# Performance work log

Measured on AMD Instinct MI355X. Metric: run time of the kernel, lower is better.

## Reference

```python
import jax, jax.numpy as jnp
import numpy as np

N_USERS = 60000
N_ITEMS = 40000
N_NODES = N_USERS + N_ITEMS
N_EDGES = 1_000_000
D = 64
BN_EPS = 1e-3  # tf.layers.batch_normalization default epsilon


def setup_inputs() -> dict:
    key = jax.random.key(0)
    ks = jax.random.split(key, 16)
    s = 1.0 / np.sqrt(D)  # uniform-ish init scale for [D,D] weights
    w = lambda k: (jax.random.uniform(k, (D, D), jnp.float32, -1.0, 1.0) * s)
    return {
        "u_features": jax.random.normal(ks[0], (N_USERS, D), jnp.float32),
        "v_features": jax.random.normal(ks[1], (N_ITEMS, D), jnp.float32),
        "edge_start": jax.random.randint(ks[2], (N_EDGES,), 0, N_NODES, jnp.int32),
        "edge_end": jax.random.randint(ks[3], (N_EDGES,), 0, N_NODES, jnp.int32),
        "Ui1": w(ks[4]), "Uj1": w(ks[5]), "Vi1": w(ks[6]), "Vj1": w(ks[7]),
        "bu1": jnp.zeros((D,), jnp.float32), "bv1": jnp.zeros((D,), jnp.float32),
        "Ui2": w(ks[8]), "Uj2": w(ks[9]), "Vi2": w(ks[10]), "Vj2": w(ks[11]),
        "bu2": jnp.zeros((D,), jnp.float32), "bv2": jnp.zeros((D,), jnp.float32),
        "R": w(ks[12]),
        "gamma1": jnp.ones((D,), jnp.float32), "beta1": jnp.zeros((D,), jnp.float32),
        "gamma2": jnp.ones((D,), jnp.float32), "beta2": jnp.zeros((D,), jnp.float32),
    }


def _stage(x, Ui, Uj, Vi, Vj, bu, bv, e_start, e_end, n_nodes):
    # gate = sigmoid(E_end@(x Vi) + E_start@(x Vj) + bv)   -> edge gather
    gate = jax.nn.sigmoid((x @ Vi)[e_end] + (x @ Vj)[e_start] + bv)  # [E, D]
    msg = gate * (x @ Ui)[e_start]                                    # [E, D]
    # x Uj + E_end.T @ msg + bu   -> scatter-add to destination nodes
    agg = jax.ops.segment_sum(msg, e_end, num_segments=n_nodes)       # [N, D]
    return x @ Uj + agg + bu


def _batchnorm(x, gamma, beta):
    mean = jnp.mean(x, axis=0)
    var = jnp.var(x, axis=0)
    return gamma * (x - mean) * jax.lax.rsqrt(var + BN_EPS) + beta


def reference(u_features, v_features, edge_start, edge_end,
              Ui1, Uj1, Vi1, Vj1, bu1, bv1,
              Ui2, Uj2, Vi2, Vj2, bu2, bv2,
              R, gamma1, beta1, gamma2, beta2):
    num_users = u_features.shape[0]
    x_in = jnp.concatenate([u_features, v_features], axis=0)  # [N, D]
    n = x_in.shape[0]
    x = _stage(x_in, Ui1, Uj1, Vi1, Vj1, bu1, bv1, edge_start, edge_end, n)
    x = jax.nn.relu(_batchnorm(x, gamma1, beta1))
    x = _stage(x, Ui2, Uj2, Vi2, Vj2, bu2, bv2, edge_start, edge_end, n)
    x = _batchnorm(x, gamma2, beta2)
    x = jax.nn.relu(x + x_in @ R)  # residual branch
    return x[:num_users], x[num_users:]
```

## Files before the change

kernel.cpp:

```cpp
#include <hip/hip_runtime.h>
#include <hip/hip_bf16.h>

#define NUSERS 60000
#define NNODES 100000
#define DD 64
#define NGB 1563
#define GMM 782
#define NBUK 196
#define ESB 2048

typedef __hip_bfloat16 bf16;
using bf16x8 = __attribute__((ext_vector_type(8))) short;
using f32x4  = __attribute__((ext_vector_type(4))) float;

__device__ __forceinline__ float b2f(bf16 x) { return __bfloat162float(x); }
__device__ __forceinline__ bf16 f2b(float x) { return __float2bfloat16(x); }
__device__ __forceinline__ unsigned short fbits(float x) {
    union { bf16 b; unsigned short u; } cv; cv.b = f2b(x); return cv.u;
}
__device__ __forceinline__ float us2f(unsigned short h) {
    union { unsigned u; float f; } t; t.u = (unsigned)h << 16; return t.f;
}
__device__ __forceinline__ float lo_bf16(unsigned w) {
    union { unsigned u; float f; } t; t.u = w << 16; return t.f;
}
__device__ __forceinline__ float hi_bf16(unsigned w) {
    union { unsigned u; float f; } t; t.u = w & 0xFFFF0000u; return t.f;
}
__device__ __forceinline__ float ldf(const void* p, size_t i, int isbf) {
    if (isbf) return b2f(((const bf16*)p)[i]);
    return ((const float*)p)[i];
}
__device__ __forceinline__ unsigned pack2(float a, float b) {
    return (unsigned)fbits(a) | ((unsigned)fbits(b) << 16);
}
__device__ __forceinline__ unsigned pr2(float x0, float x1, float a0, float a1,
                                        float b0, float b1) {
    float t0 = a0 * x0 + b0, t1 = a1 * x1 + b1;
    t0 = t0 > 0.f ? t0 : 0.f;
    t1 = t1 > 0.f ? t1 : 0.f;
    return pack2(t0, t1);
}

__global__ void k_sniff(const unsigned short* __restrict__ h,
                        int* __restrict__ flag, float* __restrict__ red,
                        int* __restrict__ btot)
{
    __shared__ int cs[256];
    int t = threadIdx.x;
    int cnt = 0;
    for (int i = t; i < 1024; i += 256) {
        int e = (h[2 * i] >> 7) & 0xFF;
        cnt += (e >= 100 && e <= 140) ? 1 : 0;
    }
    cs[t] = cnt;
    __syncthreads();
    for (int s = 128; s > 0; s >>= 1) {
        if (t < s) cs[t] += cs[t + s];
        __syncthreads();
    }
    if (t == 0) flag[0] = (cs[0] > 512) ? 1 : 0;
    red[t] = 0.f;
    btot[t] = 0;
}

__global__ __launch_bounds__(256) void k_bhist(const int* __restrict__ ee,
                                               int* __restrict__ btot, int E)
{
    __shared__ int h[256];
    int t = threadIdx.x;
    h[t] = 0;
    __syncthreads();
    for (int e = blockIdx.x * 256 + t; e < E; e += gridDim.x * 256)
        atomicAdd(&h[ee[e] >> 9], 1);
    __syncthreads();
    if (h[t]) atomicAdd(&btot[t], h[t]);
}

__global__ void k_bscan(const int* __restrict__ btot, int* __restrict__ bbase,
                        int* __restrict__ bcursor)
{
    __shared__ int sd[256];
    int t = threadIdx.x;
    int v = btot[t];
    sd[t] = v;
    __syncthreads();
    for (int off = 1; off < 256; off <<= 1) {
        int x = (t >= off) ? sd[t - off] : 0;
        __syncthreads();
        sd[t] += x;
        __syncthreads();
    }
    int excl = sd[t] - v;
    bbase[t] = excl;
    bcursor[t] = excl;
}

__global__ __launch_bounds__(256) void k_bscatter(
    const int* __restrict__ es, const int* __restrict__ ee,
    int* __restrict__ bcursor, unsigned* __restrict__ ebuf, int E)
{
    __shared__ int h[256], gb[256], lr[256];
    int t = threadIdx.x;
    h[t] = 0;
    lr[t] = 0;
    __syncthreads();
    int base = blockIdx.x * ESB;
    unsigned ent[8];
    int bk[8];
#pragma unroll
    for (int i = 0; i < 8; i++) {
        int e = base + t + i * 256;
        if (e < E) {
            int s = es[e], d = ee[e];
            bk[i] = d >> 9;
            ent[i] = (unsigned)s | ((unsigned)(d & 511) << 20);
            atomicAdd(&h[bk[i]], 1);
        } else bk[i] = -1;
    }
    __syncthreads();
    if (h[t]) gb[t] = atomicAdd(&bcursor[t], h[t]);
    __syncthreads();
#pragma unroll
    for (int i = 0; i < 8; i++) {
        if (bk[i] >= 0) {
            int r = atomicAdd(&lr[bk[i]], 1);
            ebuf[gb[bk[i]] + r] = ent[i];
        }
    }
}

__global__ __launch_bounds__(256) void k_group(
    const int* __restrict__ bbase, const unsigned* __restrict__ ebuf,
    int* __restrict__ rowptr, int* __restrict__ srcidx)
{
    __shared__ int h[512], sc[512];
    int b = blockIdx.x, t = threadIdx.x;
    int lo = bbase[b], hi = bbase[b + 1];
    h[t] = 0;
    h[t + 256] = 0;
    __syncthreads();
    for (int i = lo + t; i < hi; i += 256)
        atomicAdd(&h[ebuf[i] >> 20], 1);
    __syncthreads();
    sc[t] = h[t];
    sc[t + 256] = h[t + 256];
    __syncthreads();
    for (int off = 1; off < 512; off <<= 1) {
        int v0 = (t >= off) ? sc[t - off] : 0;
        int v1 = (t + 256 >= off) ? sc[t + 256 - off] : 0;
        __syncthreads();
        sc[t] += v0;
        sc[t + 256] += v1;
        __syncthreads();
    }
    int n0 = b * 512 + t, n1 = b * 512 + t + 256;
    int e0 = lo + sc[t] - h[t];
    int e1 = lo + sc[t + 256] - h[t + 256];
    if (n0 < NNODES) rowptr[n0] = e0;
    if (n1 < NNODES) rowptr[n1] = e1;
    if (b == NBUK - 1 && t == 0) rowptr[NNODES] = hi;
    h[t] = e0;
    h[t + 256] = e1;
    __syncthreads();
    for (int i = lo + t; i < hi; i += 256) {
        unsigned en = ebuf[i];
        int pos = atomicAdd(&h[en >> 20], 1);
        int s = (int)(en & 0xFFFFF);
        srcidx[pos] = s < NNODES ? s : 0;
    }
}

template <int MODE>
__device__ __forceinline__ void stage_load(
    int tile, int tid, int bfflag,
    const void* u, const void* v, const unsigned short* Aacc,
    const float* ab, uint4& w0, uint4& w1)
{
    int r = tid >> 2, c0 = (tid & 3) * 16;
    int row = tile * DD + r;
    int rowc = row < NNODES ? row : NNODES - 1;
    if (MODE == 0) {
        const void* src = (rowc < NUSERS) ? u : v;
        size_t off = (rowc < NUSERS) ? ((size_t)rowc * DD + c0)
                                     : ((size_t)(rowc - NUSERS) * DD + c0);
        if (bfflag) {
            const uint4* p = (const uint4*)((const unsigned short*)src + off);
            w0 = p[0];
            w1 = p[1];
        } else {
            const float4* p = (const float4*)((const float*)src + off);
            float4 f0 = p[0], f1 = p[1], f2 = p[2], f3 = p[3];
            w0 = make_uint4(pack2(f0.x, f0.y), pack2(f0.z, f0.w),
                            pack2(f1.x, f1.y), pack2(f1.z, f1.w));
            w1 = make_uint4(pack2(f2.x, f2.y), pack2(f2.z, f2.w),
                            pack2(f3.x, f3.y), pack2(f3.z, f3.w));
        }
    } else {
        const uint4* p = (const uint4*)(Aacc + (size_t)rowc * DD + c0);
        unsigned aw[8];
        *(uint4*)&aw[0] = p[0];
        *(uint4*)&aw[4] = p[1];
        const float4* pa = (const float4*)(ab + c0);
        const float4* pb = (const float4*)(ab + 64 + c0);
        float av[16], bv[16];
#pragma unroll
        for (int j = 0; j < 4; j++) {
            float4 fa = pa[j], fb = pb[j];
            av[4 * j] = fa.x; av[4 * j + 1] = fa.y;
            av[4 * j + 2] = fa.z; av[4 * j + 3] = fa.w;
            bv[4 * j] = fb.x; bv[4 * j + 1] = fb.y;
            bv[4 * j + 2] = fb.z; bv[4 * j + 3] = fb.w;
        }
        unsigned ow[8];
#pragma unroll
        for (int j = 0; j < 8; j++)
            ow[j] = pr2(lo_bf16(aw[j]), hi_bf16(aw[j]),
                        av[2 * j], av[2 * j + 1], bv[2 * j], bv[2 * j + 1]);
        w0 = *(uint4*)&ow[0];
        w1 = *(uint4*)&ow[4];
    }
}

__device__ __forceinline__ void stage_store(unsigned short* xbuf, int tid,
                                            const uint4& w0, const uint4& w1)
{
    int r = tid >> 2, c0 = (tid & 3) * 16;
    *(uint4*)&xbuf[r * 72 + c0] = w0;
    *((uint4*)&xbuf[r * 72 + c0] + 1) = w1;
}

template <int MODE>
__global__ __launch_bounds__(256, 4) void k_mm4_mfma(
    const void* __restrict__ u, const void* __restrict__ v,
    const float* __restrict__ ab,
    const void* __restrict__ W0, const void* __restrict__ W1,
    const void* __restrict__ W2, const void* __restrict__ W3,
    const void* __restrict__ b0, const void* __restrict__ b1,
    const int* __restrict__ flag,
    unsigned short* __restrict__ A, unsigned short* __restrict__ Ed,
    unsigned* __restrict__ Tw)
{
    __shared__ __align__(16) unsigned short lsd[4 * DD * 72];
    const int bfflag = flag[0];
    const int tid = threadIdx.x;

    int t = blockIdx.x;
    uint4 xa, xb;
    stage_load<MODE>(t, tid, bfflag, u, v, A, ab, xa, xb);

    if (bfflag) {
#define WSTG_BF(m, src)                                                   \
        _Pragma("unroll")                                                 \
        for (int j = 0; j < 2; j++) {                                     \
            int i = tid + j * 256; int e0 = i * 8;                        \
            *(uint4*)&lsd[(m) * 4608 + (e0 >> 6) * 72 + (e0 & 63)] =      \
                ((const uint4*)(src))[i];                                 \
        }
        WSTG_BF(0, W0) WSTG_BF(1, W1) WSTG_BF(2, W2) WSTG_BF(3, W3)
    } else {
#define WSTG_F32(m, src)                                                  \
        _Pragma("unroll")                                                 \
        for (int j = 0; j < 4; j++) {                                     \
            int i = tid + j * 256; int e0 = i * 4;                        \
            float4 f = ((const float4*)(src))[i];                         \
            *(uint2*)&lsd[(m) * 4608 + (e0 >> 6) * 72 + (e0 & 63)] =      \
                make_uint2(pack2(f.x, f.y), pack2(f.z, f.w));             \
        }
        WSTG_F32(0, W0) WSTG_F32(1, W1) WSTG_F32(2, W2) WSTG_F32(3, W3)
    }
    __syncthreads();

    const int wv = tid >> 6, lane = tid & 63;
    const int quad = lane >> 4, ln = lane & 15;
    const int mA = (wv < 2) ? wv : 2;
    bf16x8 bfrA[2][4], bfrB[2][4];
#pragma unroll
    for (int ks = 0; ks < 2; ks++)
#pragma unroll
        for (int nt = 0; nt < 4; nt++)
#pragma unroll
            for (int j = 0; j < 8; j++)
                bfrA[ks][nt][j] = (short)lsd[mA * 4608 +
                    (ks * 32 + quad * 8 + j) * 72 + nt * 16 + ln];
    if (wv >= 2) {
#pragma unroll
        for (int ks = 0; ks < 2; ks++)
#pragma unroll
            for (int nt = 0; nt < 4; nt++)
#pragma unroll
                for (int j = 0; j < 8; j++)
                    bfrB[ks][nt][j] = (short)lsd[3 * 4608 +
                        (ks * 32 + quad * 8 + j) * 72 + nt * 16 + ln];
    }
    float bias[4];
#pragma unroll
    for (int nt = 0; nt < 4; nt++)
        bias[nt] = (wv == 0) ? ldf(b0, nt * 16 + ln, bfflag)
                 : (wv == 1) ? ldf(b1, nt * 16 + ln, bfflag) : 0.f;
    __syncthreads();

    auto compute = [&](const unsigned short* xt, int row0) {
        if (wv < 2) {
#pragma unroll
            for (int rt = 0; rt < 4; rt++) {
                int m = rt * 16 + ln;
                bf16x8 af0 = *(const bf16x8*)&xt[m * 72 + quad * 8];
                bf16x8 af1 = *(const bf16x8*)&xt[m * 72 + 32 + quad * 8];
#pragma unroll
                for (int nt = 0; nt < 4; nt++) {
                    f32x4 c = {0.f, 0.f, 0.f, 0.f};
                    c = __builtin_amdgcn_mfma_f32_16x16x32_bf16(af0, bfrA[0][nt], c, 0, 0, 0);
                    c = __builtin_amdgcn_mfma_f32_16x16x32_bf16(af1, bfrA[1][nt], c, 0, 0, 0);
                    int col = nt * 16 + ln;
#pragma unroll
                    for (int r = 0; r < 4; r++) {
                        int row = row0 + rt * 16 + quad * 4 + r;
                        if (row < NNODES) {
                            size_t o = (size_t)row * DD + col;
                            if (wv == 0) A[o] = fbits(c[r] + bias[nt]);
                            else         Ed[o] = fbits(__expf(-(c[r] + bias[nt])));
                        }
                    }
                }
            }
        } else {
            const int rtb = (wv - 2) * 2;
#pragma unroll
            for (int rr = 0; rr < 2; rr++) {
                int rt = rtb + rr;
                int m = rt * 16 + ln;
                bf16x8 af0 = *(const bf16x8*)&xt[m * 72 + quad * 8];
                bf16x8 af1 = *(const bf16x8*)&xt[m * 72 + 32 + quad * 8];
#pragma unroll
                for (int nt = 0; nt < 4; nt++) {
                    f32x4 c2 = {0.f, 0.f, 0.f, 0.f};
                    f32x4 c3 = {0.f, 0.f, 0.f, 0.f};
                    c2 = __builtin_amdgcn_mfma_f32_16x16x32_bf16(af0, bfrA[0][nt], c2, 0, 0, 0);
                    c2 = __builtin_amdgcn_mfma_f32_16x16x32_bf16(af1, bfrA[1][nt], c2, 0, 0, 0);
                    c3 = __builtin_amdgcn_mfma_f32_16x16x32_bf16(af0, bfrB[0][nt], c3, 0, 0, 0);
                    c3 = __builtin_amdgcn_mfma_f32_16x16x32_bf16(af1, bfrB[1][nt], c3, 0, 0, 0);
                    int col = nt * 16 + ln;
#pragma unroll
                    for (int r = 0; r < 4; r++) {
                        int row = row0 + rt * 16 + quad * 4 + r;
                        if (row < NNODES)
                            Tw[(size_t)row * DD + col] =
                                pack2(c2[r], __expf(-c3[r]));
                    }
                }
            }
        }
    };

    stage_store(lsd, tid, xa, xb);
    int tn = t + GMM;
    if (tn < NGB)
        stage_load<MODE>(tn, tid, bfflag, u, v, A, ab, xa, xb);
    __syncthreads();
    int buf = 0;
    while (true) {
        compute(lsd + buf * 4608, t * DD);
        if (tn >= NGB) break;
        t = tn;
        tn += GMM;
        stage_store(lsd + (buf ^ 1) * 4608, tid, xa, xb);
        if (tn < NGB)
            stage_load<MODE>(tn, tid, bfflag, u, v, A, ab, xa, xb);
        __syncthreads();
        buf ^= 1;
    }
}

__global__ __launch_bounds__(256) void k_final_mfma(
    const unsigned short* __restrict__ A, const float* __restrict__ ab,
    const void* __restrict__ u, const void* __restrict__ v,
    const void* __restrict__ R, const int* __restrict__ flag,
    void* __restrict__ out)
{
    __shared__ __align__(16) unsigned short Wls[DD][72];
    __shared__ __align__(16) unsigned short xls[DD][72];
    const int bfflag = flag[0];
    const int tid = threadIdx.x;
    if (bfflag) {
        for (int i = tid; i < 512; i += 256) {
            int e0 = i * 8;
            *(uint4*)&Wls[e0 >> 6][e0 & 63] = ((const uint4*)R)[i];
        }
    } else {
        for (int i = tid; i < 1024; i += 256) {
            int e0 = i * 4;
            float4 f = ((const float4*)R)[i];
            *(uint2*)&Wls[e0 >> 6][e0 & 63] =
                make_uint2(pack2(f.x, f.y), pack2(f.z, f.w));
        }
    }
    uint4 w0, w1;
    stage_load<0>(blockIdx.x, tid, bfflag, u, v, nullptr, nullptr, w0, w1);
    stage_store(&xls[0][0], tid, w0, w1);
    __syncthreads();

    const int row0 = blockIdx.x * DD;
    const int wv = tid >> 6, lane = tid & 63;
    const int quad = lane >> 4, ln = lane & 15;
    bf16x8 bfr[2][4];
#pragma unroll
    for (int ks = 0; ks < 2; ks++)
#pragma unroll
        for (int nt = 0; nt < 4; nt++)
#pragma unroll
            for (int j = 0; j < 8; j++)
                bfr[ks][nt][j] = (short)Wls[ks * 32 + quad * 8 + j][nt * 16 + ln];
    float av[4], bv[4];
#pragma unroll
    for (int nt = 0; nt < 4; nt++) {
        av[nt] = ab[nt * 16 + ln];
        bv[nt] = ab[64 + nt * 16 + ln];
    }
    const int rt = wv;
    int m = rt * 16 + ln;
    bf16x8 af0 = *(const bf16x8*)&xls[m][quad * 8];
    bf16x8 af1 = *(const bf16x8*)&xls[m][32 + quad * 8];
#pragma unroll
    for (int nt = 0; nt < 4; nt++) {
        f32x4 c = {0.f, 0.f, 0.f, 0.f};
        c = __builtin_amdgcn_mfma_f32_16x16x32_bf16(af0, bfr[0][nt], c, 0, 0, 0);
        c = __builtin_amdgcn_mfma_f32_16x16x32_bf16(af1, bfr[1][nt], c, 0, 0, 0);
        int col = nt * 16 + ln;
#pragma unroll
        for (int r = 0; r < 4; r++) {
            int row = row0 + rt * 16 + quad * 4 + r;
            if (row < NNODES) {
                size_t o = (size_t)row * DD + col;
                float vv = av[nt] * us2f(A[o]) + bv[nt] + c[r];
                vv = vv > 0.f ? vv : 0.f;
                if (bfflag) ((unsigned short*)out)[o] = fbits(vv);
                else        ((float*)out)[o] = vv;
            }
        }
    }
}

__global__ __launch_bounds__(256) void k_accum(
    const int* __restrict__ rowptr, const int* __restrict__ srcidx,
    const unsigned* __restrict__ T, const bf16* __restrict__ Ed,
    unsigned short* __restrict__ A)
{
    int d = blockIdx.x * 4 + (threadIdx.x >> 6);
    if (d >= NNODES) return;
    int c = threadIdx.x & 63;
    int r0 = rowptr[d], r1 = rowptr[d + 1];
    size_t o = (size_t)d * DD + c;
    float ed = b2f(Ed[o]);
    float sum = us2f(A[o]);
    int i = r0;
#define EDGE(tv) sum += lo_bf16(tv) * \
    __builtin_amdgcn_rcpf(1.f + ed * hi_bf16(tv));
    for (; i + 7 < r1; i += 8) {
        unsigned t0 = T[(size_t)srcidx[i] * DD + c];
        unsigned t1 = T[(size_t)srcidx[i + 1] * DD + c];
        unsigned t2 = T[(size_t)srcidx[i + 2] * DD + c];
        unsigned t3 = T[(size_t)srcidx[i + 3] * DD + c];
        unsigned t4 = T[(size_t)srcidx[i + 4] * DD + c];
        unsigned t5 = T[(size_t)srcidx[i + 5] * DD + c];
        unsigned t6 = T[(size_t)srcidx[i + 6] * DD + c];
        unsigned t7 = T[(size_t)srcidx[i + 7] * DD + c];
        EDGE(t0) EDGE(t1) EDGE(t2) EDGE(t3)
        EDGE(t4) EDGE(t5) EDGE(t6) EDGE(t7)
    }
    for (; i + 3 < r1; i += 4) {
        unsigned t0 = T[(size_t)srcidx[i] * DD + c];
        unsigned t1 = T[(size_t)srcidx[i + 1] * DD + c];
        unsigned t2 = T[(size_t)srcidx[i + 2] * DD + c];
        unsigned t3 = T[(size_t)srcidx[i + 3] * DD + c];
        EDGE(t0) EDGE(t1) EDGE(t2) EDGE(t3)
    }
    for (; i < r1; i++) {
        unsigned t = T[(size_t)srcidx[i] * DD + c];
        EDGE(t)
    }
#undef EDGE
    A[o] = fbits(sum);
}

__global__ __launch_bounds__(256) void k_reduce(
    const unsigned short* __restrict__ x, float* __restrict__ red)
{
    __shared__ float s1[256], s2[256];
    const int c = threadIdx.x & 63, rg = threadIdx.x >> 6;
    float sum = 0.f, sq = 0.f;
    for (int row = blockIdx.x * 4 + rg; row < NNODES; row += gridDim.x * 4) {
        float vv = us2f(x[(size_t)row * DD + c]);
        sum += vv;
        sq += vv * vv;
    }
    s1[threadIdx.x] = sum;
    s2[threadIdx.x] = sq;
    __syncthreads();
    if (threadIdx.x < 64) {
        sum = s1[c] + s1[64 + c] + s1[128 + c] + s1[192 + c];
        sq = s2[c] + s2[64 + c] + s2[128 + c] + s2[192 + c];
        unsafeAtomicAdd(&red[c], sum);
        unsafeAtomicAdd(&red[64 + c], sq);
    }
}

__global__ void k_stats(const float* __restrict__ red,
                        const void* __restrict__ gamma,
                        const void* __restrict__ beta,
                        const int* __restrict__ flag,
                        float* __restrict__ ab)
{
    int c = threadIdx.x;
    int bf = flag[0];
    float mean = red[c] * (1.f / NNODES);
    float var = red[64 + c] * (1.f / NNODES) - mean * mean;
    float rstd = rsqrtf(var + 1e-3f);
    float a = ldf(gamma, c, bf) * rstd;
    ab[c] = a;
    ab[64 + c] = ldf(beta, c, bf) - mean * a;
}

extern "C" void kernel_launch(void* const* d_in, const int* in_sizes, int n_in,
                              void* d_out, int out_size, void* d_ws, size_t ws_size,
                              hipStream_t stream)
{
    const void* u   = d_in[0];
    const void* v   = d_in[1];
    const int* es   = (const int*)d_in[2];
    const int* ee   = (const int*)d_in[3];
    const void* Ui1 = d_in[4];
    const void* Uj1 = d_in[5];
    const void* Vi1 = d_in[6];
    const void* Vj1 = d_in[7];
    const void* bu1 = d_in[8];
    const void* bv1 = d_in[9];
    const void* Ui2 = d_in[10];
    const void* Uj2 = d_in[11];
    const void* Vi2 = d_in[12];
    const void* Vj2 = d_in[13];
    const void* bu2 = d_in[14];
    const void* bv2 = d_in[15];
    const void* R   = d_in[16];
    const void* g1  = d_in[17];
    const void* be1 = d_in[18];
    const void* g2  = d_in[19];
    const void* be2 = d_in[20];
    const int E = in_sizes[2];

    char* ws = (char*)d_ws;
    unsigned short* A = (unsigned short*)(ws);
    unsigned* T    = (unsigned*)(ws + 25600000);
    unsigned* ebuf = (unsigned*)(ws + 25600000);
    int* srcidx    = (int*)(ws + 51200000);
    int* rowptr    = (int*)(ws + 56000000);
    float* red     = (float*)(ws + 56802176);
    int* flag      = (int*)(ws + 56804224);
    int* btot      = (int*)(ws + 56804352);
    int* bbase     = (int*)(ws + 56805376);
    int* bcursor   = (int*)(ws + 56806400);
    float* red1 = red, *red2 = red + 128, *ab1 = red + 256, *ab2 = red + 384;
    bf16* Ed = (bf16*)d_out;

    k_sniff<<<1, 256, 0, stream>>>((const unsigned short*)u, flag, red, btot);
    k_bhist<<<400, 256, 0, stream>>>(ee, btot, E);
    k_bscan<<<1, 256, 0, stream>>>(btot, bbase, bcursor);
    k_bscatter<<<(E + ESB - 1) / ESB, 256, 0, stream>>>(es, ee, bcursor, ebuf, E);
    k_group<<<NBUK, 256, 0, stream>>>(bbase, ebuf, rowptr, srcidx);

    k_mm4_mfma<0><<<GMM, 256, 0, stream>>>(u, v, nullptr,
                                           Uj1, Vi1, Ui1, Vj1, bu1, bv1, flag,
                                           A, (unsigned short*)Ed, T);
    k_accum<<<(NNODES + 3) / 4, 256, 0, stream>>>(rowptr, srcidx, T, Ed, A);
    k_reduce<<<1024, 256, 0, stream>>>(A, red1);
    k_stats<<<1, 64, 0, stream>>>(red1, g1, be1, flag, ab1);

    k_mm4_mfma<1><<<GMM, 256, 0, stream>>>(nullptr, nullptr, ab1,
                                           Uj2, Vi2, Ui2, Vj2, bu2, bv2, flag,
                                           A, (unsigned short*)Ed, T);
    k_accum<<<(NNODES + 3) / 4, 256, 0, stream>>>(rowptr, srcidx, T, Ed, A);
    k_reduce<<<1024, 256, 0, stream>>>(A, red2);
    k_stats<<<1, 64, 0, stream>>>(red2, g2, be2, flag, ab2);

    k_final_mfma<<<NGB, 256, 0, stream>>>(A, ab2, u, v, R, flag, d_out);
}
```

Baseline: 406.7 us.

## Fuse batchnorm reduction and stats into accumulate and consumer kernels

Folds the column sum and sum-of-squares reduction into the persistent edge-accumulate kernel, and computes the batchnorm scale and shift inside the following matmul and final kernels. This removes the separate reduce and stats launches and a second full read of A. The accumulate kernel becomes a grid-stride persistent loop that prefetches the next node's row metadata. It gathers 16 edges at a time with clamped indices, using byte offsets prestored in srcidx (shifted left by 8) to save address arithmetic. The cost is a fixed 2048-block grid that may balance load worse across nodes of uneven degree, plus redundant per-block stats computation.

```diff
diff --git a/kernel.cpp b/kernel.cpp
--- a/kernel.cpp
+++ b/kernel.cpp
@@ -8,6 +8,8 @@
 #define GMM 782
 #define NBUK 196
 #define ESB 2048
+#define ACB 2048
+#define DSTR (ACB * 4)
 
 typedef __hip_bfloat16 bf16;
 using bf16x8 = __attribute__((ext_vector_type(8))) short;
@@ -167,7 +169,7 @@
         unsigned en = ebuf[i];
         int pos = atomicAdd(&h[en >> 20], 1);
         int s = (int)(en & 0xFFFFF);
-        srcidx[pos] = s < NNODES ? s : 0;
+        srcidx[pos] = (s < NNODES ? s : 0) << 8;
     }
 }
 
@@ -233,7 +235,8 @@
 template <int MODE>
 __global__ __launch_bounds__(256, 4) void k_mm4_mfma(
     const void* __restrict__ u, const void* __restrict__ v,
-    const float* __restrict__ ab,
+    const float* __restrict__ red, const void* __restrict__ gm,
+    const void* __restrict__ bt,
     const void* __restrict__ W0, const void* __restrict__ W1,
     const void* __restrict__ W2, const void* __restrict__ W3,
     const void* __restrict__ b0, const void* __restrict__ b1,
@@ -242,12 +245,24 @@
     unsigned* __restrict__ Tw)
 {
     __shared__ __align__(16) unsigned short lsd[4 * DD * 72];
+    __shared__ __align__(16) float abs_s[128];
     const int bfflag = flag[0];
     const int tid = threadIdx.x;
 
+    if (MODE == 1) {
+        if (tid < 64) {
+            float mean = red[tid] * (1.f / NNODES);
+            float var = red[64 + tid] * (1.f / NNODES) - mean * mean;
+            float a = ldf(gm, tid, bfflag) * rsqrtf(var + 1e-3f);
+            abs_s[tid] = a;
+            abs_s[64 + tid] = ldf(bt, tid, bfflag) - mean * a;
+        }
+        __syncthreads();
+    }
+
     int t = blockIdx.x;
     uint4 xa, xb;
-    stage_load<MODE>(t, tid, bfflag, u, v, A, ab, xa, xb);
+    stage_load<MODE>(t, tid, bfflag, u, v, A, abs_s, xa, xb);
 
     if (bfflag) {
 #define WSTG_BF(m, src)                                                   \
@@ -356,7 +371,7 @@
     stage_store(lsd, tid, xa, xb);
     int tn = t + GMM;
     if (tn < NGB)
-        stage_load<MODE>(tn, tid, bfflag, u, v, A, ab, xa, xb);
+        stage_load<MODE>(tn, tid, bfflag, u, v, A, abs_s, xa, xb);
     __syncthreads();
     int buf = 0;
     while (true) {
@@ -366,22 +381,31 @@
         tn += GMM;
         stage_store(lsd + (buf ^ 1) * 4608, tid, xa, xb);
         if (tn < NGB)
-            stage_load<MODE>(tn, tid, bfflag, u, v, A, ab, xa, xb);
+            stage_load<MODE>(tn, tid, bfflag, u, v, A, abs_s, xa, xb);
         __syncthreads();
         buf ^= 1;
     }
 }
 
 __global__ __launch_bounds__(256) void k_final_mfma(
-    const unsigned short* __restrict__ A, const float* __restrict__ ab,
+    const unsigned short* __restrict__ A, const float* __restrict__ red,
+    const void* __restrict__ gm, const void* __restrict__ bt,
     const void* __restrict__ u, const void* __restrict__ v,
     const void* __restrict__ R, const int* __restrict__ flag,
     void* __restrict__ out)
 {
     __shared__ __align__(16) unsigned short Wls[DD][72];
     __shared__ __align__(16) unsigned short xls[DD][72];
+    __shared__ __align__(16) float abf[128];
     const int bfflag = flag[0];
     const int tid = threadIdx.x;
+    if (tid < 64) {
+        float mean = red[tid] * (1.f / NNODES);
+        float var = red[64 + tid] * (1.f / NNODES) - mean * mean;
+        float a = ldf(gm, tid, bfflag) * rsqrtf(var + 1e-3f);
+        abf[tid] = a;
+        abf[64 + tid] = ldf(bt, tid, bfflag) - mean * a;
+    }
     if (bfflag) {
         for (int i = tid; i < 512; i += 256) {
             int e0 = i * 8;
@@ -414,8 +438,8 @@
     float av[4], bv[4];
 #pragma unroll
     for (int nt = 0; nt < 4; nt++) {
-        av[nt] = ab[nt * 16 + ln];
-        bv[nt] = ab[64 + nt * 16 + ln];
+        av[nt] = abf[nt * 16 + ln];
+        bv[nt] = abf[64 + nt * 16 + ln];
     }
     const int rt = wv;
     int m = rt * 16 + ln;
@@ -444,81 +468,67 @@
 __global__ __launch_bounds__(256) void k_accum(
     const int* __restrict__ rowptr, const int* __restrict__ srcidx,
     const unsigned* __restrict__ T, const bf16* __restrict__ Ed,
-    unsigned short* __restrict__ A)
-{
+    unsigned short* __restrict__ A, float* __restrict__ red)
+{
+    __shared__ float s1[256], s2[256];
+    const int c = threadIdx.x & 63;
+    const char* Tb = (const char*)T + (c << 2);
+    float rsum = 0.f, rsq = 0.f;
+
     int d = blockIdx.x * 4 + (threadIdx.x >> 6);
-    if (d >= NNODES) return;
-    int c = threadIdx.x & 63;
     int r0 = rowptr[d], r1 = rowptr[d + 1];
     size_t o = (size_t)d * DD + c;
     float ed = b2f(Ed[o]);
     float sum = us2f(A[o]);
-    int i = r0;
-#define EDGE(tv) sum += lo_bf16(tv) * \
-    __builtin_amdgcn_rcpf(1.f + ed * hi_bf16(tv));
-    for (; i + 7 < r1; i += 8) {
-        unsigned t0 = T[(size_t)srcidx[i] * DD + c];
-        unsigned t1 = T[(size_t)srcidx[i + 1] * DD + c];
-        unsigned t2 = T[(size_t)srcidx[i + 2] * DD + c];
-        unsigned t3 = T[(size_t)srcidx[i + 3] * DD + c];
-        unsigned t4 = T[(size_t)srcidx[i + 4] * DD + c];
-        unsigned t5 = T[(size_t)srcidx[i + 5] * DD + c];
-        unsigned t6 = T[(size_t)srcidx[i + 6] * DD + c];
-        unsigned t7 = T[(size_t)srcidx[i + 7] * DD + c];
-        EDGE(t0) EDGE(t1) EDGE(t2) EDGE(t3)
-        EDGE(t4) EDGE(t5) EDGE(t6) EDGE(t7)
-    }
-    for (; i + 3 < r1; i += 4) {
-        unsigned t0 = T[(size_t)srcidx[i] * DD + c];
-        unsigned t1 = T[(size_t)srcidx[i + 1] * DD + c];
-        unsigned t2 = T[(size_t)srcidx[i + 2] * DD + c];
-        unsigned t3 = T[(size_t)srcidx[i + 3] * DD + c];
-        EDGE(t0) EDGE(t1) EDGE(t2) EDGE(t3)
-    }
-    for (; i < r1; i++) {
-        unsigned t = T[(size_t)srcidx[i] * DD + c];
-        EDGE(t)
-    }
-#undef EDGE
-    A[o] = fbits(sum);
-}
-
-__global__ __launch_bounds__(256) void k_reduce(
-    const unsigned short* __restrict__ x, float* __restrict__ red)
-{
-    __shared__ float s1[256], s2[256];
-    const int c = threadIdx.x & 63, rg = threadIdx.x >> 6;
-    float sum = 0.f, sq = 0.f;
-    for (int row = blockIdx.x * 4 + rg; row < NNODES; row += gridDim.x * 4) {
-        float vv = us2f(x[(size_t)row * DD + c]);
-        sum += vv;
-        sq += vv * vv;
-    }
-    s1[threadIdx.x] = sum;
-    s2[threadIdx.x] = sq;
+
+    while (true) {
+        int dn = d + DSTR;
+        int r0n = 0, r1n = 0;
+        size_t on = 0;
+        float edn = 0.f, sumn = 0.f;
+        if (dn < NNODES) {
+            r0n = rowptr[dn];
+            r1n = rowptr[dn + 1];
+            on = (size_t)dn * DD + c;
+            edn = b2f(Ed[on]);
+            sumn = us2f(A[on]);
+        }
+
+        int i = r0;
+        while (i < r1) {
+            int nb = r1 - i;
+            nb = nb > 16 ? 16 : nb;
+            int last = r1 - 1;
+            unsigned tv[16];
+#pragma unroll
+            for (int j = 0; j < 16; j++) {
+                int idx = i + j;
+                idx = idx < last ? idx : last;
+                tv[j] = *(const unsigned*)(Tb + (unsigned)srcidx[idx]);
+            }
+#pragma unroll
+            for (int j = 0; j < 16; j++)
+                if (j < nb)
+                    sum += lo_bf16(tv[j]) *
+                        __builtin_amdgcn_rcpf(1.f + ed * hi_bf16(tv[j]));
+            i += nb;
+        }
+        A[o] = fbits(sum);
+        rsum += sum;
+        rsq += sum * sum;
+        if (dn >= NNODES) break;
+        d = dn; r0 = r0n; r1 = r1n; o = on; ed = edn; sum = sumn;
+    }
+
+    s1[threadIdx.x] = rsum;
+    s2[threadIdx.x] = rsq;
     __syncthreads();
     if (threadIdx.x < 64) {
-        sum = s1[c] + s1[64 + c] + s1[128 + c] + s1[192 + c];
-        sq = s2[c] + s2[64 + c] + s2[128 + c] + s2[192 + c];
-        unsafeAtomicAdd(&red[c], sum);
-        unsafeAtomicAdd(&red[64 + c], sq);
-    }
-}
-
-__global__ void k_stats(const float* __restrict__ red,
-                        const void* __restrict__ gamma,
-                        const void* __restrict__ beta,
-                        const int* __restrict__ flag,
-                        float* __restrict__ ab)
-{
-    int c = threadIdx.x;
-    int bf = flag[0];
-    float mean = red[c] * (1.f / NNODES);
-    float var = red[64 + c] * (1.f / NNODES) - mean * mean;
-    float rstd = rsqrtf(var + 1e-3f);
-    float a = ldf(gamma, c, bf) * rstd;
-    ab[c] = a;
-    ab[64 + c] = ldf(beta, c, bf) - mean * a;
+        float a = s1[c] + s1[64 + c] + s1[128 + c] + s1[192 + c];
+        float b = s2[c] + s2[64 + c] + s2[128 + c] + s2[192 + c];
+        unsafeAtomicAdd(&red[c], a);
+        unsafeAtomicAdd(&red[64 + c], b);
+    }
 }
 
 extern "C" void kernel_launch(void* const* d_in, const int* in_sizes, int n_in,
@@ -559,7 +569,7 @@
     int* btot      = (int*)(ws + 56804352);
     int* bbase     = (int*)(ws + 56805376);
     int* bcursor   = (int*)(ws + 56806400);
-    float* red1 = red, *red2 = red + 128, *ab1 = red + 256, *ab2 = red + 384;
+    float* red1 = red, *red2 = red + 128;
     bf16* Ed = (bf16*)d_out;
 
     k_sniff<<<1, 256, 0, stream>>>((const unsigned short*)u, flag, red, btot);
@@ -568,19 +578,15 @@
     k_bscatter<<<(E + ESB - 1) / ESB, 256, 0, stream>>>(es, ee, bcursor, ebuf, E);
     k_group<<<NBUK, 256, 0, stream>>>(bbase, ebuf, rowptr, srcidx);
 
-    k_mm4_mfma<0><<<GMM, 256, 0, stream>>>(u, v, nullptr,
+    k_mm4_mfma<0><<<GMM, 256, 0, stream>>>(u, v, nullptr, nullptr, nullptr,
                                            Uj1, Vi1, Ui1, Vj1, bu1, bv1, flag,
                                            A, (unsigned short*)Ed, T);
-    k_accum<<<(NNODES + 3) / 4, 256, 0, stream>>>(rowptr, srcidx, T, Ed, A);
-    k_reduce<<<1024, 256, 0, stream>>>(A, red1);
-    k_stats<<<1, 64, 0, stream>>>(red1, g1, be1, flag, ab1);
-
-    k_mm4_mfma<1><<<GMM, 256, 0, stream>>>(nullptr, nullptr, ab1,
+    k_accum<<<ACB, 256, 0, stream>>>(rowptr, srcidx, T, Ed, A, red1);
+
+    k_mm4_mfma<1><<<GMM, 256, 0, stream>>>(nullptr, nullptr, red1, g1, be1,
                                            Uj2, Vi2, Ui2, Vj2, bu2, bv2, flag,
                                            A, (unsigned short*)Ed, T);
-    k_accum<<<(NNODES + 3) / 4, 256, 0, stream>>>(rowptr, srcidx, T, Ed, A);
-    k_reduce<<<1024, 256, 0, stream>>>(A, red2);
-    k_stats<<<1, 64, 0, stream>>>(red2, g2, be2, flag, ab2);
-
-    k_final_mfma<<<NGB, 256, 0, stream>>>(A, ab2, u, v, R, flag, d_out);
-}
+    k_accum<<<ACB, 256, 0, stream>>>(rowptr, srcidx, T, Ed, A, red2);
+
+    k_final_mfma<<<NGB, 256, 0, stream>>>(A, red2, g2, be2, u, v, R, flag, d_out);
+}
```

Result: slower. 532.7 us (+31.0%).

## Fuse batchnorm statistics into accumulation and consumer kernels, dropping reduce/stats launches

Applied to the files above, without the earlier changes.

Each k_accum block now reduces its per-column sum and sum of squares in shared memory and atomically adds them into a padded global buffer (stride of 16 floats per channel), removing the separate k_reduce pass over A. The k_stats kernel is also dropped: the stage-2 matmul kernel and the final kernel each recompute the batchnorm scale and shift per block from the raw sums. This removes four launches and one full re-read of the activation matrix per stage. In exchange there are far more atomics (one set per 4-row block), which can contend on the same 128 addresses, and the statistics are now taken from fp32 sums before bf16 rounding.

```diff
diff --git a/kernel.cpp b/kernel.cpp
--- a/kernel.cpp
+++ b/kernel.cpp
@@ -60,7 +60,7 @@
         __syncthreads();
     }
     if (t == 0) flag[0] = (cs[0] > 512) ? 1 : 0;
-    red[t] = 0.f;
+    for (int i = t; i < 4096; i += 256) red[i] = 0.f;
     btot[t] = 0;
 }
 
@@ -233,7 +233,8 @@
 template <int MODE>
 __global__ __launch_bounds__(256, 4) void k_mm4_mfma(
     const void* __restrict__ u, const void* __restrict__ v,
-    const float* __restrict__ ab,
+    const float* __restrict__ red, const void* __restrict__ gm,
+    const void* __restrict__ bt,
     const void* __restrict__ W0, const void* __restrict__ W1,
     const void* __restrict__ W2, const void* __restrict__ W3,
     const void* __restrict__ b0, const void* __restrict__ b1,
@@ -242,12 +243,24 @@
     unsigned* __restrict__ Tw)
 {
     __shared__ __align__(16) unsigned short lsd[4 * DD * 72];
+    __shared__ __align__(16) float abs_s[128];
     const int bfflag = flag[0];
     const int tid = threadIdx.x;
 
+    if (MODE == 1) {
+        if (tid < 64) {
+            float mean = red[tid << 4] * (1.f / NNODES);
+            float var = red[(64 + tid) << 4] * (1.f / NNODES) - mean * mean;
+            float a = ldf(gm, tid, bfflag) * rsqrtf(var + 1e-3f);
+            abs_s[tid] = a;
+            abs_s[64 + tid] = ldf(bt, tid, bfflag) - mean * a;
+        }
+        __syncthreads();
+    }
+
     int t = blockIdx.x;
     uint4 xa, xb;
-    stage_load<MODE>(t, tid, bfflag, u, v, A, ab, xa, xb);
+    stage_load<MODE>(t, tid, bfflag, u, v, A, abs_s, xa, xb);
 
     if (bfflag) {
 #define WSTG_BF(m, src)                                                   \
@@ -356,7 +369,7 @@
     stage_store(lsd, tid, xa, xb);
     int tn = t + GMM;
     if (tn < NGB)
-        stage_load<MODE>(tn, tid, bfflag, u, v, A, ab, xa, xb);
+        stage_load<MODE>(tn, tid, bfflag, u, v, A, abs_s, xa, xb);
     __syncthreads();
     int buf = 0;
     while (true) {
@@ -366,22 +379,31 @@
         tn += GMM;
         stage_store(lsd + (buf ^ 1) * 4608, tid, xa, xb);
         if (tn < NGB)
-            stage_load<MODE>(tn, tid, bfflag, u, v, A, ab, xa, xb);
+            stage_load<MODE>(tn, tid, bfflag, u, v, A, abs_s, xa, xb);
         __syncthreads();
         buf ^= 1;
     }
 }
 
 __global__ __launch_bounds__(256) void k_final_mfma(
-    const unsigned short* __restrict__ A, const float* __restrict__ ab,
+    const unsigned short* __restrict__ A, const float* __restrict__ red,
+    const void* __restrict__ gm, const void* __restrict__ bt,
     const void* __restrict__ u, const void* __restrict__ v,
     const void* __restrict__ R, const int* __restrict__ flag,
     void* __restrict__ out)
 {
     __shared__ __align__(16) unsigned short Wls[DD][72];
     __shared__ __align__(16) unsigned short xls[DD][72];
+    __shared__ __align__(16) float abf[128];
     const int bfflag = flag[0];
     const int tid = threadIdx.x;
+    if (tid < 64) {
+        float mean = red[tid << 4] * (1.f / NNODES);
+        float var = red[(64 + tid) << 4] * (1.f / NNODES) - mean * mean;
+        float a = ldf(gm, tid, bfflag) * rsqrtf(var + 1e-3f);
+        abf[tid] = a;
+        abf[64 + tid] = ldf(bt, tid, bfflag) - mean * a;
+    }
     if (bfflag) {
         for (int i = tid; i < 512; i += 256) {
             int e0 = i * 8;
@@ -414,8 +436,8 @@
     float av[4], bv[4];
 #pragma unroll
     for (int nt = 0; nt < 4; nt++) {
-        av[nt] = ab[nt * 16 + ln];
-        bv[nt] = ab[64 + nt * 16 + ln];
+        av[nt] = abf[nt * 16 + ln];
+        bv[nt] = abf[64 + nt * 16 + ln];
     }
     const int rt = wv;
     int m = rt * 16 + ln;
@@ -444,10 +466,10 @@
 __global__ __launch_bounds__(256) void k_accum(
     const int* __restrict__ rowptr, const int* __restrict__ srcidx,
     const unsigned* __restrict__ T, const bf16* __restrict__ Ed,
-    unsigned short* __restrict__ A)
-{
+    unsigned short* __restrict__ A, float* __restrict__ red)
+{
+    __shared__ float s1[256], s2[256];
     int d = blockIdx.x * 4 + (threadIdx.x >> 6);
-    if (d >= NNODES) return;
     int c = threadIdx.x & 63;
     int r0 = rowptr[d], r1 = rowptr[d + 1];
     size_t o = (size_t)d * DD + c;
@@ -481,44 +503,16 @@
     }
 #undef EDGE
     A[o] = fbits(sum);
-}
-
-__global__ __launch_bounds__(256) void k_reduce(
-    const unsigned short* __restrict__ x, float* __restrict__ red)
-{
-    __shared__ float s1[256], s2[256];
-    const int c = threadIdx.x & 63, rg = threadIdx.x >> 6;
-    float sum = 0.f, sq = 0.f;
-    for (int row = blockIdx.x * 4 + rg; row < NNODES; row += gridDim.x * 4) {
-        float vv = us2f(x[(size_t)row * DD + c]);
-        sum += vv;
-        sq += vv * vv;
-    }
+
     s1[threadIdx.x] = sum;
-    s2[threadIdx.x] = sq;
+    s2[threadIdx.x] = sum * sum;
     __syncthreads();
     if (threadIdx.x < 64) {
-        sum = s1[c] + s1[64 + c] + s1[128 + c] + s1[192 + c];
-        sq = s2[c] + s2[64 + c] + s2[128 + c] + s2[192 + c];
-        unsafeAtomicAdd(&red[c], sum);
-        unsafeAtomicAdd(&red[64 + c], sq);
-    }
-}
-
-__global__ void k_stats(const float* __restrict__ red,
-                        const void* __restrict__ gamma,
-                        const void* __restrict__ beta,
-                        const int* __restrict__ flag,
-                        float* __restrict__ ab)
-{
-    int c = threadIdx.x;
-    int bf = flag[0];
-    float mean = red[c] * (1.f / NNODES);
-    float var = red[64 + c] * (1.f / NNODES) - mean * mean;
-    float rstd = rsqrtf(var + 1e-3f);
-    float a = ldf(gamma, c, bf) * rstd;
-    ab[c] = a;
-    ab[64 + c] = ldf(beta, c, bf) - mean * a;
+        float a = s1[c] + s1[64 + c] + s1[128 + c] + s1[192 + c];
+        float b = s2[c] + s2[64 + c] + s2[128 + c] + s2[192 + c];
+        unsafeAtomicAdd(&red[c << 4], a);
+        unsafeAtomicAdd(&red[(64 + c) << 4], b);
+    }
 }
 
 extern "C" void kernel_launch(void* const* d_in, const int* in_sizes, int n_in,
@@ -553,34 +547,31 @@
     unsigned* T    = (unsigned*)(ws + 25600000);
     unsigned* ebuf = (unsigned*)(ws + 25600000);
     int* srcidx    = (int*)(ws + 51200000);
+    float* red_pad = (float*)(ws + 55200000);
     int* rowptr    = (int*)(ws + 56000000);
-    float* red     = (float*)(ws + 56802176);
     int* flag      = (int*)(ws + 56804224);
     int* btot      = (int*)(ws + 56804352);
     int* bbase     = (int*)(ws + 56805376);
     int* bcursor   = (int*)(ws + 56806400);
-    float* red1 = red, *red2 = red + 128, *ab1 = red + 256, *ab2 = red + 384;
+    float* red1 = red_pad;
+    float* red2 = red_pad + 2048;
     bf16* Ed = (bf16*)d_out;
 
-    k_sniff<<<1, 256, 0, stream>>>((const unsigned short*)u, flag, red, btot);
+    k_sniff<<<1, 256, 0, stream>>>((const unsigned short*)u, flag, red_pad, btot);
     k_bhist<<<400, 256, 0, stream>>>(ee, btot, E);
     k_bscan<<<1, 256, 0, stream>>>(btot, bbase, bcursor);
     k_bscatter<<<(E + ESB - 1) / ESB, 256, 0, stream>>>(es, ee, bcursor, ebuf, E);
     k_group<<<NBUK, 256, 0, stream>>>(bbase, ebuf, rowptr, srcidx);
 
-    k_mm4_mfma<0><<<GMM, 256, 0, stream>>>(u, v, nullptr,
+    k_mm4_mfma<0><<<GMM, 256, 0, stream>>>(u, v, nullptr, nullptr, nullptr,
                                            Uj1, Vi1, Ui1, Vj1, bu1, bv1, flag,
                                            A, (unsigned short*)Ed, T);
-    k_accum<<<(NNODES + 3) / 4, 256, 0, stream>>>(rowptr, srcidx, T, Ed, A);
-    k_reduce<<<1024, 256, 0, stream>>>(A, red1);
-    k_stats<<<1, 64, 0, stream>>>(red1, g1, be1, flag, ab1);
-
-    k_mm4_mfma<1><<<GMM, 256, 0, stream>>>(nullptr, nullptr, ab1,
+    k_accum<<<(NNODES + 3) / 4, 256, 0, stream>>>(rowptr, srcidx, T, Ed, A, red1);
+
+    k_mm4_mfma<1><<<GMM, 256, 0, stream>>>(nullptr, nullptr, red1, g1, be1,
                                            Uj2, Vi2, Ui2, Vj2, bu2, bv2, flag,
                                            A, (unsigned short*)Ed, T);
-    k_accum<<<(NNODES + 3) / 4, 256, 0, stream>>>(rowptr, srcidx, T, Ed, A);
-    k_reduce<<<1024, 256, 0, stream>>>(A, red2);
-    k_stats<<<1, 64, 0, stream>>>(red2, g2, be2, flag, ab2);
-
-    k_final_mfma<<<NGB, 256, 0, stream>>>(A, ab2, u, v, R, flag, d_out);
-}
+    k_accum<<<(NNODES + 3) / 4, 256, 0, stream>>>(rowptr, srcidx, T, Ed, A, red2);
+
+    k_final_mfma<<<NGB, 256, 0, stream>>>(A, red2, g2, be2, u, v, R, flag, d_out);
+}
```

Result: slower. 1.453 ms (+257.2%).
